# Kernel optimization log

Hardware: AMD Instinct MI355X
Metric: run time of the kernel (lower is better)

The kernel has to match this reference:

```python
import jax, jax.numpy as jnp
import numpy as np

HIDDEN = 2048
N_HEADS = 16
HEAD_DIM = HIDDEN // N_HEADS  # 128
ROTARY_DIM = 32
ROPE_BASE = 10000.0
NEG_INF = -10000.0  # matches torch code's additive mask constant


def setup_inputs() -> dict:
    key = jax.random.key(0)
    k1, k2, k3 = jax.random.split(key, 3)
    x = jax.random.normal(k1, (2, 2048, HIDDEN), dtype=jnp.float32)
    # scale weights like nn.Linear default init (uniform ~ 1/sqrt(fan_in))
    Wqkv_w = jax.random.normal(k2, (3 * HIDDEN, HIDDEN), dtype=jnp.float32) * (1.0 / np.sqrt(HIDDEN))
    Wqkv_b = jax.random.normal(k3, (3 * HIDDEN,), dtype=jnp.float32) * 0.01
    return {"x": x, "Wqkv_w": Wqkv_w, "Wqkv_b": Wqkv_b}


def _rope_cos_sin(seqlen, dtype):
    inv_freq = 1.0 / (ROPE_BASE ** (jnp.arange(0, ROTARY_DIM, 2, dtype=jnp.float32) / ROTARY_DIM))
    t = jnp.arange(seqlen, dtype=jnp.float32)
    freqs = jnp.outer(t, inv_freq)  # (S, ROTARY_DIM//2)
    return jnp.cos(freqs).astype(dtype), jnp.sin(freqs).astype(dtype)


def _apply_rotary(u, cos, sin):
    # u: (B, S, H, D); rotate first ROTARY_DIM dims, GPT-NeoX half-split style
    u_rot, u_pass = u[..., :ROTARY_DIM], u[..., ROTARY_DIM:]
    u1, u2 = u_rot[..., : ROTARY_DIM // 2], u_rot[..., ROTARY_DIM // 2 :]
    c = cos[None, :, None, :]  # (1, S, 1, ROTARY_DIM//2)
    s = sin[None, :, None, :]
    rot = jnp.concatenate([u1 * c - u2 * s, u1 * s + u2 * c], axis=-1)
    return jnp.concatenate([rot, u_pass], axis=-1)


def reference(x, Wqkv_w, Wqkv_b):
    B, S, _ = x.shape
    qkv = jnp.einsum("bse,oe->bso", x, Wqkv_w) + Wqkv_b  # (B, S, 3*H*D)
    qkv = qkv.reshape(B, S, 3, N_HEADS, HEAD_DIM)
    cos, sin = _rope_cos_sin(S, x.dtype)
    q = _apply_rotary(qkv[:, :, 0], cos, sin)
    k = _apply_rotary(qkv[:, :, 1], cos, sin)
    v = qkv[:, :, 2]
    scale = 1.0 / np.sqrt(HEAD_DIM)
    scores = jnp.einsum("bthd,bshd->bhts", q, k * scale)  # (B, H, T, S)
    causal_mask = jnp.triu(jnp.full((S, S), NEG_INF, dtype=scores.dtype), 1)
    scores = scores + causal_mask
    attn = jax.nn.softmax(scores, axis=-1)
    out = jnp.einsum("bhts,bshd->bthd", attn, v)  # (B, S, H, D)
    return out.reshape(B, S, N_HEADS * HEAD_DIM)
```

## Files before the change

kernel.cpp:

```cpp
#include <hip/hip_runtime.h>

#define B_    2
#define S_    2048
#define E_    2048
#define NH_   16
#define HD_   128
#define NQKV_ 6144
#define M_    4096
#define XN_   (M_ * E_)
#define NPAN  (E_ / 32)

typedef short bf16x8 __attribute__((ext_vector_type(8)));
typedef float f32x4  __attribute__((ext_vector_type(4)));

typedef const __attribute__((address_space(1))) void* gas_t;
typedef __attribute__((address_space(3))) void*       las_t;

__device__ inline float b2f(unsigned short u) {
    return __uint_as_float(((unsigned int)u) << 16);
}
__device__ inline unsigned short f2b(float f) {
    unsigned int x = __float_as_uint(f);
    x = x + 0x7fffu + ((x >> 16) & 1u);
    return (unsigned short)(x >> 16);
}
__device__ inline unsigned int pk2(float lo, float hi) {
    return (unsigned int)f2b(lo) | ((unsigned int)f2b(hi) << 16);
}

__global__ __launch_bounds__(256) void cvt_bf16(
    const float* __restrict__ X,
    const float* __restrict__ W,
    unsigned short* __restrict__ O)
{
    const long i = (long)(blockIdx.x * 256 + threadIdx.x) * 8;
    const float* src = (i < XN_) ? (X + i) : (W + (i - XN_));
    const float4 a = *(const float4*)(src);
    const float4 b = *(const float4*)(src + 4);
    uint4 o = { pk2(a.x, a.y), pk2(a.z, a.w), pk2(b.x, b.y), pk2(b.z, b.w) };
    *(uint4*)(O + i) = o;
}

__global__ __launch_bounds__(512, 4) void qkv_gemm(
    const unsigned short* __restrict__ Xb,
    const unsigned short* __restrict__ Wb,
    const float* __restrict__ bias,
    unsigned short* __restrict__ qb,
    unsigned short* __restrict__ kb,
    unsigned short* __restrict__ vb)
{
    __shared__ __align__(16) unsigned short As[3][128 * 32];
    __shared__ __align__(16) unsigned short Bs[3][256 * 32];

    const int t    = threadIdx.x;
    const int lane = t & 63;
    const int w    = t >> 6;
    const int wr   = w >> 2;
    const int wc   = w & 3;
    const int quad = (lane >> 4) & 3;
    const int l16  = lane & 15;

    const int wg = ((int)blockIdx.x & 7) * 96 + ((int)blockIdx.x >> 3);
    const int m0 = (wg / 24) * 128;
    const int n0 = (wg % 24) * 256;

    auto stageA = [&](int p) {
        const int sl = p % 3;
        const int k0 = p * 32;
        const int ub  = w * 64;
        const int u   = ub + lane;
        const int row = u >> 2;
        const int ko  = (u & 3) ^ ((row >> 1) & 3);
        __builtin_amdgcn_global_load_lds(
            (gas_t)(Xb + (size_t)(m0 + row) * E_ + k0 + ko * 8),
            (las_t)&As[sl][ub * 8], 16, 0, 0);
    };
    auto stageB = [&](int p) {
        const int sl = p % 3;
        const int k0 = p * 32;
        #pragma unroll
        for (int c = 0; c < 2; c++) {
            const int ub  = c * 512 + w * 64;
            const int u   = ub + lane;
            const int row = u >> 2;
            const int ko  = (u & 3) ^ ((row >> 1) & 3);
            __builtin_amdgcn_global_load_lds(
                (gas_t)(Wb + (size_t)(n0 + row) * E_ + k0 + ko * 8),
                (las_t)&Bs[sl][ub * 8], 16, 0, 0);
        }
    };

    f32x4 acc[4][4];
    #pragma unroll
    for (int i = 0; i < 4; i++)
        #pragma unroll
        for (int j = 0; j < 4; j++)
            #pragma unroll
            for (int r = 0; r < 4; r++) acc[i][j][r] = 0.0f;

    stageA(0); stageB(0);
    stageA(1); stageB(1);
    asm volatile("s_waitcnt vmcnt(0)" ::: "memory");
    __builtin_amdgcn_s_barrier();

    for (int p = 0; p < NPAN; p++) {
        const int sl = p % 3;
        bf16x8 af[4], bfv[4];

        #pragma unroll
        for (int mf = 0; mf < 4; mf++) {
            const int row = wr * 64 + mf * 16 + l16;
            af[mf] = *(const bf16x8*)&As[sl][row * 32 + (quad ^ ((row >> 1) & 3)) * 8];
        }
        #pragma unroll
        for (int nf = 0; nf < 4; nf++) {
            const int rb = wc * 64 + nf * 16 + l16;
            bfv[nf] = *(const bf16x8*)&Bs[sl][rb * 32 + (quad ^ ((rb >> 1) & 3)) * 8];
        }

        if (p + 2 < NPAN) {
            stageA(p + 2); stageB(p + 2);
            asm volatile("s_waitcnt vmcnt(3)" ::: "memory");
        } else {
            asm volatile("s_waitcnt vmcnt(0)" ::: "memory");
        }
        __builtin_amdgcn_s_barrier();
        __builtin_amdgcn_s_setprio(1);
        #pragma unroll
        for (int mf = 0; mf < 4; mf++)
            #pragma unroll
            for (int nf = 0; nf < 4; nf++)
                acc[mf][nf] = __builtin_amdgcn_mfma_f32_16x16x32_bf16(
                    af[mf], bfv[nf], acc[mf][nf], 0, 0, 0);
        __builtin_amdgcn_s_setprio(0);
        __builtin_amdgcn_s_barrier();
    }

    const int which = n0 >> 11;
    unsigned short* dst = (which == 0) ? qb : ((which == 1) ? kb : vb);

    float bv[4];
    #pragma unroll
    for (int nf = 0; nf < 4; nf++) bv[nf] = bias[n0 + wc * 64 + nf * 16 + l16];
    #pragma unroll
    for (int mi = 0; mi < 4; mi++)
        #pragma unroll
        for (int nf = 0; nf < 4; nf++)
            #pragma unroll
            for (int r = 0; r < 4; r++) acc[mi][nf][r] += bv[nf];

    if ((wc & 1) == 0 && which < 2) {
        const float inv = exp2f(-0.83048202372184059f * (float)l16);
        #pragma unroll
        for (int mi = 0; mi < 4; mi++) {
            #pragma unroll
            for (int r = 0; r < 4; r++) {
                const int m = m0 + wr * 64 + mi * 16 + quad * 4 + r;
                const int sdx = m & (S_ - 1);
                float c, sn;
                __sincosf((float)sdx * inv, &sn, &c);
                const float u1 = acc[mi][0][r], u2 = acc[mi][1][r];
                acc[mi][0][r] = u1 * c - u2 * sn;
                acc[mi][1][r] = u1 * sn + u2 * c;
            }
        }
    }

    #pragma unroll
    for (int nf = 0; nf < 4; nf++) {
        const int hh = ((n0 + wc * 64 + nf * 16) >> 7) & 15;
        const int d  = ((wc * 64 + nf * 16) & 127) + l16;
        #pragma unroll
        for (int mi = 0; mi < 4; mi++) {
            #pragma unroll
            for (int r = 0; r < 4; r++) {
                const int m   = m0 + wr * 64 + mi * 16 + quad * 4 + r;
                const int bb  = m >> 11;
                const int sdx = m & (S_ - 1);
                dst[((size_t)(bb * NH_ + hh) * S_ + sdx) * HD_ + d] =
                    f2b(acc[mi][nf][r]);
            }
        }
    }
}

#define KSTR 128
#define VSTR 72
#define PSTR 72
#define OSTR 132

__global__ __launch_bounds__(256, 3) void attn_mfma(
    const unsigned short* __restrict__ qb,
    const unsigned short* __restrict__ kb,
    const unsigned short* __restrict__ vb,
    float* __restrict__ out)
{
    union SM {
        struct {
            unsigned short Ks[64 * KSTR];
            unsigned short Vt[128 * VSTR];
            unsigned short Ps[4 * 16 * PSTR];
        } a;
        float Ow[4 * 16 * OSTR];
    };
    __shared__ __align__(16) SM sm;
    unsigned short* Ks = sm.a.Ks;
    unsigned short* Vt = sm.a.Vt;
    unsigned short* Ps = sm.a.Ps;

    const int bid  = blockIdx.x;
    const int qt   = 31 - (bid >> 5);
    const int bh   = bid & 31;
    const int b    = bh >> 4;
    const int h    = bh & 15;
    const int t    = threadIdx.x;
    const int lane = t & 63;
    const int w    = t >> 6;
    const int quad = lane >> 4;
    const int l16  = lane & 15;

    const int wrow0  = qt * 64 + w * 16;
    const int ntiles = qt + 1;

    unsigned short* Pw = Ps + w * 16 * PSTR;

    const int krow = t >> 2, kub = (t & 3) * 4;
    const int vq   = t & 31, vd0 = (t >> 5) * 16;

    bf16x8 qf[4];
    {
        const unsigned short* qp =
            qb + ((size_t)(bh * S_ + wrow0 + l16)) * HD_ + quad * 8;
        #pragma unroll
        for (int c = 0; c < 4; c++)
            qf[c] = *(const bf16x8*)(qp + c * 32);
    }

    f32x4 of[8];
    #pragma unroll
    for (int db = 0; db < 8; db++)
        #pragma unroll
        for (int r = 0; r < 4; r++) of[db][r] = 0.0f;
    float mr[4], lr[4];
    #pragma unroll
    for (int r = 0; r < 4; r++) { mr[r] = -1e30f; lr[r] = 0.0f; }

    const float scale2 = 0.12751744459892879f;
    const float mneg2  = -14426.950408889634f;

    uint4 kr[4];
    uint4 v0a, v0b, v1a, v1b;

    auto issue_tile = [&](int kt2) {
        const int s2 = kt2 * 64;
        const unsigned short* kg = kb + ((size_t)(bh * S_ + s2 + krow)) * HD_ + kub * 8;
        #pragma unroll
        for (int u = 0; u < 4; u++) kr[u] = *(const uint4*)(kg + u * 8);
        const unsigned short* vg = vb + ((size_t)(bh * S_ + s2 + 2 * vq)) * HD_ + vd0;
        v0a = *(const uint4*)(vg);
        v0b = *(const uint4*)(vg + 8);
        v1a = *(const uint4*)(vg + HD_);
        v1b = *(const uint4*)(vg + HD_ + 8);
    };

    issue_tile(0);

    for (int kt = 0; kt < ntiles; kt++) {
        const int s0 = kt * 64;
        __syncthreads();
        #pragma unroll
        for (int u = 0; u < 4; u++) {
            const int unit = (kub + u) ^ (krow & 7);
            *(uint4*)&Ks[krow * KSTR + unit * 8] = kr[u];
        }
        {
            unsigned int r0[8] = { v0a.x, v0a.y, v0a.z, v0a.w,
                                   v0b.x, v0b.y, v0b.z, v0b.w };
            unsigned int r1[8] = { v1a.x, v1a.y, v1a.z, v1a.w,
                                   v1b.x, v1b.y, v1b.z, v1b.w };
            #pragma unroll
            for (int j = 0; j < 16; j++) {
                const int u = j >> 1;
                unsigned int pk;
                if ((j & 1) == 0)
                    pk = (r0[u] & 0xffffu) | (r1[u] << 16);
                else
                    pk = (r0[u] >> 16) | (r1[u] & 0xffff0000u);
                *(unsigned int*)&Vt[(vd0 + j) * VSTR + 2 * vq] = pk;
            }
        }
        __syncthreads();

        if (kt + 1 < ntiles) issue_tile(kt + 1);

        f32x4 sf[4];
        #pragma unroll
        for (int nb = 0; nb < 4; nb++)
            #pragma unroll
            for (int r = 0; r < 4; r++) sf[nb][r] = 0.0f;
        #pragma unroll
        for (int c = 0; c < 4; c++) {
            #pragma unroll
            for (int nb = 0; nb < 4; nb++) {
                const int unit = (4 * c + quad) ^ (l16 & 7);
                bf16x8 kf = *(const bf16x8*)&Ks[(nb * 16 + l16) * KSTR + unit * 8];
                sf[nb] = __builtin_amdgcn_mfma_f32_16x16x32_bf16(
                    qf[c], kf, sf[nb], 0, 0, 0);
            }
        }

        const bool need_mask = (s0 + 63 > wrow0);
        {
            const int qr0 = wrow0 + quad * 4;
            #pragma unroll
            for (int nb = 0; nb < 4; nb++) {
                const int kcol = s0 + nb * 16 + l16;
                #pragma unroll
                for (int r = 0; r < 4; r++) {
                    float s = sf[nb][r] * scale2;
                    if (need_mask && kcol > qr0 + r) s += mneg2;
                    sf[nb][r] = s;
                }
            }
        }

        {
            float mt4[4];
            #pragma unroll
            for (int r = 0; r < 4; r++) {
                float mt = fmaxf(fmaxf(sf[0][r], sf[1][r]),
                                 fmaxf(sf[2][r], sf[3][r]));
                mt = fmaxf(mt, __shfl_xor(mt, 1));
                mt = fmaxf(mt, __shfl_xor(mt, 2));
                mt = fmaxf(mt, __shfl_xor(mt, 4));
                mt = fmaxf(mt, __shfl_xor(mt, 8));
                mt4[r] = mt;
            }
            const bool grew = (mt4[0] > mr[0]) || (mt4[1] > mr[1]) ||
                              (mt4[2] > mr[2]) || (mt4[3] > mr[3]);
            if (__any(grew)) {
                float alpha[4];
                #pragma unroll
                for (int r = 0; r < 4; r++) {
                    const float mnew = fmaxf(mr[r], mt4[r]);
                    alpha[r] = __builtin_amdgcn_exp2f(mr[r] - mnew);
                    mr[r] = mnew;
                    lr[r] *= alpha[r];
                }
                #pragma unroll
                for (int db = 0; db < 8; db++)
                    #pragma unroll
                    for (int r = 0; r < 4; r++) of[db][r] *= alpha[r];
            }
            #pragma unroll
            for (int r = 0; r < 4; r++) {
                float rs = 0.0f;
                #pragma unroll
                for (int nb = 0; nb < 4; nb++) {
                    float p = __builtin_amdgcn_exp2f(sf[nb][r] - mr[r]);
                    sf[nb][r] = p;
                    rs += p;
                }
                lr[r] += rs;
            }

            #pragma unroll
            for (int nb = 0; nb < 4; nb++)
                #pragma unroll
                for (int r = 0; r < 4; r++)
                    Pw[(quad * 4 + r) * PSTR + nb * 16 + l16] = f2b(sf[nb][r]);
        }

        #pragma unroll
        for (int kc = 0; kc < 2; kc++) {
            bf16x8 pf = *(const bf16x8*)&Pw[l16 * PSTR + kc * 32 + quad * 8];
            #pragma unroll
            for (int db = 0; db < 8; db++) {
                bf16x8 vf = *(const bf16x8*)&Vt[(db * 16 + l16) * VSTR + kc * 32 + quad * 8];
                of[db] = __builtin_amdgcn_mfma_f32_16x16x32_bf16(
                    pf, vf, of[db], 0, 0, 0);
            }
        }
    }

    float* Ow = sm.Ow + w * 16 * OSTR;
    __syncthreads();
    float inv[4];
    #pragma unroll
    for (int r = 0; r < 4; r++) {
        float ls = lr[r];
        ls += __shfl_xor(ls, 1);
        ls += __shfl_xor(ls, 2);
        ls += __shfl_xor(ls, 4);
        ls += __shfl_xor(ls, 8);
        inv[r] = 1.0f / ls;
    }
    #pragma unroll
    for (int db = 0; db < 8; db++)
        #pragma unroll
        for (int r = 0; r < 4; r++)
            Ow[(quad * 4 + r) * OSTR + db * 16 + l16] = of[db][r] * inv[r];
    #pragma unroll
    for (int rg = 0; rg < 4; rg++) {
        const int rowl = rg * 4 + quad;
        float* op = out + ((size_t)(b * S_ + wrow0 + rowl)) * E_ + h * HD_;
        #pragma unroll
        for (int u = 0; u < 2; u++) {
            float4 v4 = *(const float4*)&Ow[rowl * OSTR + u * 64 + l16 * 4];
            *(float4*)(op + u * 64 + l16 * 4) = v4;
        }
    }
}

extern "C" void kernel_launch(void* const* d_in, const int* in_sizes, int n_in,
                              void* d_out, int out_size, void* d_ws, size_t ws_size,
                              hipStream_t stream)
{
    const float* x    = (const float*)d_in[0];
    const float* W    = (const float*)d_in[1];
    const float* bias = (const float*)d_in[2];
    float* out = (float*)d_out;

    const size_t per = (size_t)B_ * NH_ * S_ * HD_;
    unsigned short* qb = (unsigned short*)d_ws;
    unsigned short* kb = qb + per;
    unsigned short* vb = kb + per;
    unsigned short* Xb = vb + per;
    unsigned short* Wb = Xb + (size_t)XN_;

    const int cvt_elems = XN_ + NQKV_ * E_;
    cvt_bf16<<<cvt_elems / (256 * 8), 256, 0, stream>>>(x, W, Xb);

    dim3 gemm_grid((M_ / 128) * (NQKV_ / 256));
    qkv_gemm<<<gemm_grid, 512, 0, stream>>>(Xb, Wb, bias, qb, kb, vb);

    attn_mfma<<<dim3(32 * 32), 256, 0, stream>>>(qb, kb, vb, out);
}
```

Before: 368.6 us.

## Write V transposed from GEMM epilogue and double-buffer K/V via direct-to-LDS loads

Result: faster. 345.4 us (-6.3%).

```diff
diff --git a/kernel.cpp b/kernel.cpp
--- a/kernel.cpp
+++ b/kernel.cpp
@@ -47,10 +47,17 @@
     const float* __restrict__ bias,
     unsigned short* __restrict__ qb,
     unsigned short* __restrict__ kb,
-    unsigned short* __restrict__ vb)
+    unsigned short* __restrict__ vt)
 {
-    __shared__ __align__(16) unsigned short As[3][128 * 32];
-    __shared__ __align__(16) unsigned short Bs[3][256 * 32];
+    union GS {
+        struct {
+            unsigned short As[3][128 * 32];
+            unsigned short Bs[3][256 * 32];
+        } s;
+        unsigned short Eqk[128 * 264];
+        unsigned short Ev [256 * 136];
+    };
+    __shared__ __align__(16) GS gs;
 
     const int t    = threadIdx.x;
     const int lane = t & 63;
@@ -73,7 +80,7 @@
         const int ko  = (u & 3) ^ ((row >> 1) & 3);
         __builtin_amdgcn_global_load_lds(
             (gas_t)(Xb + (size_t)(m0 + row) * E_ + k0 + ko * 8),
-            (las_t)&As[sl][ub * 8], 16, 0, 0);
+            (las_t)&gs.s.As[sl][ub * 8], 16, 0, 0);
     };
     auto stageB = [&](int p) {
         const int sl = p % 3;
@@ -86,7 +93,7 @@
             const int ko  = (u & 3) ^ ((row >> 1) & 3);
             __builtin_amdgcn_global_load_lds(
                 (gas_t)(Wb + (size_t)(n0 + row) * E_ + k0 + ko * 8),
-                (las_t)&Bs[sl][ub * 8], 16, 0, 0);
+                (las_t)&gs.s.Bs[sl][ub * 8], 16, 0, 0);
         }
     };
 
@@ -110,12 +117,12 @@
         #pragma unroll
         for (int mf = 0; mf < 4; mf++) {
             const int row = wr * 64 + mf * 16 + l16;
-            af[mf] = *(const bf16x8*)&As[sl][row * 32 + (quad ^ ((row >> 1) & 3)) * 8];
+            af[mf] = *(const bf16x8*)&gs.s.As[sl][row * 32 + (quad ^ ((row >> 1) & 3)) * 8];
         }
         #pragma unroll
         for (int nf = 0; nf < 4; nf++) {
             const int rb = wc * 64 + nf * 16 + l16;
-            bfv[nf] = *(const bf16x8*)&Bs[sl][rb * 32 + (quad ^ ((rb >> 1) & 3)) * 8];
+            bfv[nf] = *(const bf16x8*)&gs.s.Bs[sl][rb * 32 + (quad ^ ((rb >> 1) & 3)) * 8];
         }
 
         if (p + 2 < NPAN) {
@@ -137,7 +144,6 @@
     }
 
     const int which = n0 >> 11;
-    unsigned short* dst = (which == 0) ? qb : ((which == 1) ? kb : vb);
 
     float bv[4];
     #pragma unroll
@@ -166,47 +172,83 @@
         }
     }
 
-    #pragma unroll
-    for (int nf = 0; nf < 4; nf++) {
-        const int hh = ((n0 + wc * 64 + nf * 16) >> 7) & 15;
-        const int d  = ((wc * 64 + nf * 16) & 127) + l16;
+    const int hb = (n0 >> 7) & 15;
+    const int bb = m0 >> 11;
+    const int sb = m0 & (S_ - 1);
+    if (which < 2) {
+        unsigned short* dst = (which == 0) ? qb : kb;
+        unsigned short* E = gs.Eqk;
         #pragma unroll
         for (int mi = 0; mi < 4; mi++) {
-            #pragma unroll
-            for (int r = 0; r < 4; r++) {
-                const int m   = m0 + wr * 64 + mi * 16 + quad * 4 + r;
-                const int bb  = m >> 11;
-                const int sdx = m & (S_ - 1);
-                dst[((size_t)(bb * NH_ + hh) * S_ + sdx) * HD_ + d] =
-                    f2b(acc[mi][nf][r]);
-            }
-        }
-    }
-}
-
-#define KSTR 128
-#define VSTR 72
+            const int m = wr * 64 + mi * 16 + quad * 4;
+            #pragma unroll
+            for (int nf = 0; nf < 4; nf++) {
+                const int col = wc * 64 + nf * 16 + l16;
+                #pragma unroll
+                for (int r = 0; r < 4; r++)
+                    E[(m + r) * 264 + col] = f2b(acc[mi][nf][r]);
+            }
+        }
+        __syncthreads();
+        const int em  = t >> 2;
+        const int ecg = (t & 3) * 8;
+        unsigned short* orow =
+            dst + ((size_t)(bb * NH_ + hb) * S_ + sb + em) * HD_;
+        #pragma unroll
+        for (int i = 0; i < 8; i++) {
+            const int chunk = ecg + i;
+            const int hh = chunk >> 4;
+            const int d  = (chunk & 15) * 8;
+            uint4 vv = *(const uint4*)&E[em * 264 + chunk * 8];
+            *(uint4*)&orow[(size_t)hh * (HD_ * S_) + d] = vv;
+        }
+    } else {
+        unsigned short* E = gs.Ev;
+        #pragma unroll
+        for (int mi = 0; mi < 4; mi++) {
+            const int m = wr * 64 + mi * 16 + quad * 4;
+            #pragma unroll
+            for (int nf = 0; nf < 4; nf++) {
+                const int col = wc * 64 + nf * 16 + l16;
+                #pragma unroll
+                for (int r = 0; r < 4; r++)
+                    E[col * 136 + m + r] = f2b(acc[mi][nf][r]);
+            }
+        }
+        __syncthreads();
+        const int col = t >> 1;
+        const int cb  = (t & 1) * 8;
+        const int hh  = hb + (col >> 7);
+        const int d   = col & 127;
+        unsigned short* vrow =
+            vt + ((size_t)(bb * NH_ + hh) * HD_ + d) * S_ + sb;
+        #pragma unroll
+        for (int i = 0; i < 8; i++) {
+            const int chunk = cb + i;
+            uint4 vv = *(const uint4*)&E[col * 136 + chunk * 8];
+            *(uint4*)&vrow[chunk * 8] = vv;
+        }
+    }
+}
+
 #define PSTR 72
 #define OSTR 132
 
-__global__ __launch_bounds__(256, 3) void attn_mfma(
+__global__ __launch_bounds__(256, 2) void attn_mfma(
     const unsigned short* __restrict__ qb,
     const unsigned short* __restrict__ kb,
-    const unsigned short* __restrict__ vb,
+    const unsigned short* __restrict__ vt,
     float* __restrict__ out)
 {
     union SM {
         struct {
-            unsigned short Ks[64 * KSTR];
-            unsigned short Vt[128 * VSTR];
+            unsigned short Ks[2][64 * 128];
+            unsigned short Vs[2][128 * 64];
             unsigned short Ps[4 * 16 * PSTR];
         } a;
         float Ow[4 * 16 * OSTR];
     };
     __shared__ __align__(16) SM sm;
-    unsigned short* Ks = sm.a.Ks;
-    unsigned short* Vt = sm.a.Vt;
-    unsigned short* Ps = sm.a.Ps;
 
     const int bid  = blockIdx.x;
     const int qt   = 31 - (bid >> 5);
@@ -222,10 +264,32 @@
     const int wrow0  = qt * 64 + w * 16;
     const int ntiles = qt + 1;
 
-    unsigned short* Pw = Ps + w * 16 * PSTR;
-
-    const int krow = t >> 2, kub = (t & 3) * 4;
-    const int vq   = t & 31, vd0 = (t >> 5) * 16;
+    unsigned short* Pw = sm.a.Ps + w * 16 * PSTR;
+
+    const int ksrow = w * 4 + (lane >> 4);
+    const int ksu   = lane & 15;
+    const int vdrow = w * 8 + (lane >> 3);
+    const int vsu   = lane & 7;
+
+    auto stage = [&](int kt2, int bsel) {
+        const int s2 = kt2 * 64;
+        #pragma unroll
+        for (int c = 0; c < 4; c++) {
+            const int srow = c * 16 + ksrow;
+            __builtin_amdgcn_global_load_lds(
+                (gas_t)(kb + ((size_t)(bh * S_ + s2 + srow)) * HD_
+                        + (ksu ^ (srow & 7)) * 8),
+                (las_t)&sm.a.Ks[bsel][(c * 16 + w * 4) * 128], 16, 0, 0);
+        }
+        #pragma unroll
+        for (int c = 0; c < 4; c++) {
+            const int drow = c * 32 + vdrow;
+            __builtin_amdgcn_global_load_lds(
+                (gas_t)(vt + ((size_t)(bh * HD_ + drow)) * S_ + s2
+                        + (vsu ^ (drow & 7)) * 8),
+                (las_t)&sm.a.Vs[bsel][(c * 32 + w * 8) * 64], 16, 0, 0);
+        }
+    };
 
     bf16x8 qf[4];
     {
@@ -248,50 +312,13 @@
     const float scale2 = 0.12751744459892879f;
     const float mneg2  = -14426.950408889634f;
 
-    uint4 kr[4];
-    uint4 v0a, v0b, v1a, v1b;
-
-    auto issue_tile = [&](int kt2) {
-        const int s2 = kt2 * 64;
-        const unsigned short* kg = kb + ((size_t)(bh * S_ + s2 + krow)) * HD_ + kub * 8;
-        #pragma unroll
-        for (int u = 0; u < 4; u++) kr[u] = *(const uint4*)(kg + u * 8);
-        const unsigned short* vg = vb + ((size_t)(bh * S_ + s2 + 2 * vq)) * HD_ + vd0;
-        v0a = *(const uint4*)(vg);
-        v0b = *(const uint4*)(vg + 8);
-        v1a = *(const uint4*)(vg + HD_);
-        v1b = *(const uint4*)(vg + HD_ + 8);
-    };
-
-    issue_tile(0);
+    stage(0, 0);
+    __syncthreads();
+    int cur = 0;
 
     for (int kt = 0; kt < ntiles; kt++) {
         const int s0 = kt * 64;
-        __syncthreads();
-        #pragma unroll
-        for (int u = 0; u < 4; u++) {
-            const int unit = (kub + u) ^ (krow & 7);
-            *(uint4*)&Ks[krow * KSTR + unit * 8] = kr[u];
-        }
-        {
-            unsigned int r0[8] = { v0a.x, v0a.y, v0a.z, v0a.w,
-                                   v0b.x, v0b.y, v0b.z, v0b.w };
-            unsigned int r1[8] = { v1a.x, v1a.y, v1a.z, v1a.w,
-                                   v1b.x, v1b.y, v1b.z, v1b.w };
-            #pragma unroll
-            for (int j = 0; j < 16; j++) {
-                const int u = j >> 1;
-                unsigned int pk;
-                if ((j & 1) == 0)
-                    pk = (r0[u] & 0xffffu) | (r1[u] << 16);
-                else
-                    pk = (r0[u] >> 16) | (r1[u] & 0xffff0000u);
-                *(unsigned int*)&Vt[(vd0 + j) * VSTR + 2 * vq] = pk;
-            }
-        }
-        __syncthreads();
-
-        if (kt + 1 < ntiles) issue_tile(kt + 1);
+        if (kt + 1 < ntiles) stage(kt + 1, cur ^ 1);
 
         f32x4 sf[4];
         #pragma unroll
@@ -302,8 +329,9 @@
         for (int c = 0; c < 4; c++) {
             #pragma unroll
             for (int nb = 0; nb < 4; nb++) {
-                const int unit = (4 * c + quad) ^ (l16 & 7);
-                bf16x8 kf = *(const bf16x8*)&Ks[(nb * 16 + l16) * KSTR + unit * 8];
+                const int u = (c * 4 + quad) ^ (l16 & 7);
+                bf16x8 kf = *(const bf16x8*)
+                    &sm.a.Ks[cur][(nb * 16 + l16) * 128 + u * 8];
                 sf[nb] = __builtin_amdgcn_mfma_f32_16x16x32_bf16(
                     qf[c], kf, sf[nb], 0, 0, 0);
             }
@@ -376,15 +404,19 @@
             bf16x8 pf = *(const bf16x8*)&Pw[l16 * PSTR + kc * 32 + quad * 8];
             #pragma unroll
             for (int db = 0; db < 8; db++) {
-                bf16x8 vf = *(const bf16x8*)&Vt[(db * 16 + l16) * VSTR + kc * 32 + quad * 8];
+                const int u = (kc * 4 + quad) ^ (l16 & 7);
+                bf16x8 vf = *(const bf16x8*)
+                    &sm.a.Vs[cur][(db * 16 + l16) * 64 + u * 8];
                 of[db] = __builtin_amdgcn_mfma_f32_16x16x32_bf16(
                     pf, vf, of[db], 0, 0, 0);
             }
         }
+
+        __syncthreads();
+        cur ^= 1;
     }
 
     float* Ow = sm.Ow + w * 16 * OSTR;
-    __syncthreads();
     float inv[4];
     #pragma unroll
     for (int r = 0; r < 4; r++) {
@@ -424,15 +456,15 @@
     const size_t per = (size_t)B_ * NH_ * S_ * HD_;
     unsigned short* qb = (unsigned short*)d_ws;
     unsigned short* kb = qb + per;
-    unsigned short* vb = kb + per;
-    unsigned short* Xb = vb + per;
+    unsigned short* vt = kb + per;
+    unsigned short* Xb = vt + per;
     unsigned short* Wb = Xb + (size_t)XN_;
 
     const int cvt_elems = XN_ + NQKV_ * E_;
     cvt_bf16<<<cvt_elems / (256 * 8), 256, 0, stream>>>(x, W, Xb);
 
     dim3 gemm_grid((M_ / 128) * (NQKV_ / 256));
-    qkv_gemm<<<gemm_grid, 512, 0, stream>>>(Xb, Wb, bias, qb, kb, vb);
-
-    attn_mfma<<<dim3(32 * 32), 256, 0, stream>>>(qb, kb, vb, out);
-}
+    qkv_gemm<<<gemm_grid, 512, 0, stream>>>(Xb, Wb, bias, qb, kb, vt);
+
+    attn_mfma<<<dim3(32 * 32), 256, 0, stream>>>(qb, kb, vt, out);
+}
```
